# Optimization experiments

Hardware: AMD Instinct MI355X
Metric: run time of the kernel (lower is better)

The kernel has to match this reference:

```python
import jax, jax.numpy as jnp
import numpy as np

N, F, B, D = 16384, 256, 48, 8


def setup_inputs() -> dict:
    key = jax.random.key(0)
    k_x, k_e, k_w, k_b = jax.random.split(key, 4)
    x = jax.random.normal(k_x, (N, F), dtype=jnp.float32)
    # per-feature sorted bin boundaries -> left edges and positive widths
    boundaries = jnp.sort(jax.random.uniform(k_e, (F, B + 1), dtype=jnp.float32,
                                             minval=-3.0, maxval=3.0), axis=-1)
    edges = boundaries[:, :-1]                     # [F, B]
    width = jnp.diff(boundaries, axis=-1)          # [F, B], > 0
    bound = 1.0 / np.sqrt(B)                       # nn.Linear default init
    W = jax.random.uniform(k_w, (F, B, D), dtype=jnp.float32, minval=-bound, maxval=bound)
    b = jax.random.uniform(k_b, (F, D), dtype=jnp.float32, minval=-bound, maxval=bound)
    return {"x": x, "edges": edges, "width": width, "W": W, "b": b}


def reference(x, edges, width, W, b):
    # piecewise-linear encoding: [N, F, B]
    h = (x[:, :, None] - edges) / width
    h = jnp.concatenate([
        jnp.minimum(h[..., :1], 1.0),          # first bin: clamp_max(1)
        jnp.clip(h[..., 1:-1], 0.0, 1.0),      # middle bins: clamp(0, 1)
        jnp.maximum(h[..., -1:], 0.0),         # last bin: clamp_min(0)
    ], axis=-1)
    # per-feature tiny Linear(B -> D), then concat over features
    out = jnp.einsum('nfb,fbd->nfd', h, W) + b   # [N, F, D]
    return out.reshape(x.shape[0], -1)           # [N, F*D]
```

## Files before the change

### kernel.cpp

```cpp
#include <hip/hip_runtime.h>


#define NN 16384
#define FF 256
#define BB 48
#define DD 8

#define FT 8
#define NSPLIT 64
#define NPB (NN / NSPLIT)

#define ESTR 52
#define RASTR 100
#define CSTR 396

__global__ __launch_bounds__(256, 6)
void cple_kernel(const float* __restrict__ X,
                 const float* __restrict__ Edg,
                 const float* __restrict__ Wid,
                 const float* __restrict__ W,
                 const float* __restrict__ Bias,
                 float* __restrict__ Out)
{
    __shared__ float sE [FT * ESTR];
    __shared__ float sRA[FT * RASTR];
    __shared__ float sC [FT * CSTR];

    const int tid = threadIdx.x;
    const int f0  = blockIdx.x * FT;
    const int ns  = blockIdx.y;

    if (tid < FT * BB / 4) {
        const float4* E4 = (const float4*)(Edg + (size_t)f0 * BB);
        float4 v = E4[tid];
        int f = tid / 12, j4 = tid % 12;
        *(float4*)&sE[f * ESTR + j4 * 4] = v;
    }
    for (int idx = tid; idx < FT * BB; idx += 256) {
        int f = idx / BB, j = idx - f * BB;
        float e = Edg[(size_t)f0 * BB + idx];
        float w = Wid[(size_t)f0 * BB + idx];
        float r = 1.0f / w;
        sRA[f * RASTR + 2 * j]     = r;
        sRA[f * RASTR + 2 * j + 1] = -e * r;
    }
    {
        const float4* Wt4 = (const float4*)(W + (size_t)f0 * BB * DD);
        #pragma unroll
        for (int q = 0; q < 3; ++q) {
            int idx4 = tid + q * 256;
            float4 v = Wt4[idx4];
            int idx = idx4 * 4;
            int f   = idx / (BB * DD);
            int rem = idx - f * (BB * DD);
            *(float4*)&sC[f * CSTR + DD + rem] = v;
        }
    }
    __syncthreads();

    const int f_l = tid & 7;
    const int n_l = tid >> 3;
    const float* eF  = &sE [f_l * ESTR];
    const float* raF = &sRA[f_l * RASTR];
    const float* cF  = &sC [f_l * CSTR];
    float c4[11];
    #pragma unroll
    for (int m = 0; m < 11; ++m) c4[m] = eF[4 * (m + 1)];

    if (tid < FT * DD) {
        int f = tid >> 3, d = tid & 7;
        float* c = &sC[f * CSTR + d];
        float acc = Bias[(size_t)(f0 + f) * DD + d];
        c[0] = acc;
        #pragma unroll
        for (int ch = 0; ch < 3; ++ch) {
            float w[16];
            #pragma unroll
            for (int j = 0; j < 16; ++j) w[j] = c[(ch * 16 + j + 1) * DD];
            #pragma unroll
            for (int j = 0; j < 16; ++j) { acc += w[j]; c[(ch * 16 + j + 1) * DD] = acc; }
        }
    }
    __syncthreads();

    const float* xp = X + (f0 + f_l);
    float* op = Out + (size_t)(f0 + f_l) * DD;

    const int nbase = ns * NPB + n_l;
    float xa = xp[(size_t)nbase * FF];
    float xb = xp[(size_t)(nbase + 128) * FF];

    #pragma unroll
    for (int i = 0; i < 4; ++i) {
        int na = nbase + i * 32;
        int nb = na + 128;
        float xA = xa, xB = xb;
        if (i < 3) {
            xa = xp[(size_t)(na + 32) * FF];
            xb = xp[(size_t)(na + 160) * FF];
        }

        int ga = 0, gb = 0;
        #pragma unroll
        for (int m = 0; m < 11; ++m) {
            ga += (xA >= c4[m]) ? 1 : 0;
            gb += (xB >= c4[m]) ? 1 : 0;
        }
        int k4a = ga * 4, k4b = gb * 4;

        float4 ea = *(const float4*)(eF + k4a);
        float4 eb = *(const float4*)(eF + k4b);
        int ka = k4a + (xA >= ea.y) + (xA >= ea.z) + (xA >= ea.w);
        int kb = k4b + (xB >= eb.y) + (xB >= eb.z) + (xB >= eb.w);

        float2 raA = *(const float2*)(raF + 2 * ka);
        float2 raB = *(const float2*)(raF + 2 * kb);
        const float* cKa = cF + ka * DD;
        const float* cKb = cF + kb * DD;
        float4 la0 = *(const float4*)(cKa);
        float4 la1 = *(const float4*)(cKa + 4);
        float4 ha0 = *(const float4*)(cKa + 8);
        float4 ha1 = *(const float4*)(cKa + 12);
        float4 lb0 = *(const float4*)(cKb);
        float4 lb1 = *(const float4*)(cKb + 4);
        float4 hb0 = *(const float4*)(cKb + 8);
        float4 hb1 = *(const float4*)(cKb + 12);

        float ta = fmaf(xA, raA.x, raA.y);
        float tb = fmaf(xB, raB.x, raB.y);

        float4 oa0, oa1, ob0, ob1;
        oa0.x = fmaf(ta, ha0.x - la0.x, la0.x);
        oa0.y = fmaf(ta, ha0.y - la0.y, la0.y);
        oa0.z = fmaf(ta, ha0.z - la0.z, la0.z);
        oa0.w = fmaf(ta, ha0.w - la0.w, la0.w);
        oa1.x = fmaf(ta, ha1.x - la1.x, la1.x);
        oa1.y = fmaf(ta, ha1.y - la1.y, la1.y);
        oa1.z = fmaf(ta, ha1.z - la1.z, la1.z);
        oa1.w = fmaf(ta, ha1.w - la1.w, la1.w);
        ob0.x = fmaf(tb, hb0.x - lb0.x, lb0.x);
        ob0.y = fmaf(tb, hb0.y - lb0.y, lb0.y);
        ob0.z = fmaf(tb, hb0.z - lb0.z, lb0.z);
        ob0.w = fmaf(tb, hb0.w - lb0.w, lb0.w);
        ob1.x = fmaf(tb, hb1.x - lb1.x, lb1.x);
        ob1.y = fmaf(tb, hb1.y - lb1.y, lb1.y);
        ob1.z = fmaf(tb, hb1.z - lb1.z, lb1.z);
        ob1.w = fmaf(tb, hb1.w - lb1.w, lb1.w);

        float4* oA = (float4*)(op + (size_t)na * (FF * DD));
        float4* oB = (float4*)(op + (size_t)nb * (FF * DD));
        oA[0] = oa0; oA[1] = oa1;
        oB[0] = ob0; oB[1] = ob1;
    }
}

extern "C" void kernel_launch(void* const* d_in, const int* in_sizes, int n_in,
                              void* d_out, int out_size, void* d_ws, size_t ws_size,
                              hipStream_t stream) {
    const float* x     = (const float*)d_in[0];
    const float* edges = (const float*)d_in[1];
    const float* width = (const float*)d_in[2];
    const float* W     = (const float*)d_in[3];
    const float* b     = (const float*)d_in[4];
    float* out = (float*)d_out;

    dim3 grid(FF / FT, NSPLIT);
    cple_kernel<<<grid, 256, 0, stream>>>(x, edges, width, W, b, out);
}
```

Measured before the change: 163.8 us.

## Split each row's 8 outputs across thread pairs and hoist x prefetch before barrier

Each (row, feature) output of 8 floats is now split between two adjacent threads, each writing one float4, so a wavefront's stores cover contiguous 16-byte chunks per lane instead of two float4s per lane. This halves the per-thread LDS table reads and FMAs but doubles the loop trip count and makes the bin search redundant across each thread pair. The first x loads are also issued before the first barrier so their latency overlaps the shared-memory setup.

```diff
diff --git a/kernel.cpp b/kernel.cpp
--- a/kernel.cpp
+++ b/kernel.cpp
@@ -56,10 +56,20 @@
             *(float4*)&sC[f * CSTR + DD + rem] = v;
         }
     }
+
+    const int h   = tid & 1;
+    const int f_l = (tid >> 1) & 7;
+    const int n_l = tid >> 4;
+
+    const float* xp = X + (f0 + f_l);
+    float* op = Out + (size_t)(f0 + f_l) * DD + h * 4;
+
+    const int nbase = ns * NPB + n_l;
+    float xa = xp[(size_t)nbase * FF];
+    float xb = xp[(size_t)(nbase + 128) * FF];
+
     __syncthreads();
 
-    const int f_l = tid & 7;
-    const int n_l = tid >> 3;
     const float* eF  = &sE [f_l * ESTR];
     const float* raF = &sRA[f_l * RASTR];
     const float* cF  = &sC [f_l * CSTR];
@@ -83,21 +93,14 @@
     }
     __syncthreads();
 
-    const float* xp = X + (f0 + f_l);
-    float* op = Out + (size_t)(f0 + f_l) * DD;
-
-    const int nbase = ns * NPB + n_l;
-    float xa = xp[(size_t)nbase * FF];
-    float xb = xp[(size_t)(nbase + 128) * FF];
-
     #pragma unroll
-    for (int i = 0; i < 4; ++i) {
-        int na = nbase + i * 32;
+    for (int i = 0; i < 8; ++i) {
+        int na = nbase + i * 16;
         int nb = na + 128;
         float xA = xa, xB = xb;
-        if (i < 3) {
-            xa = xp[(size_t)(na + 32) * FF];
-            xb = xp[(size_t)(na + 160) * FF];
+        if (i < 7) {
+            xa = xp[(size_t)(na + 16) * FF];
+            xb = xp[(size_t)(nb + 16) * FF];
         }
 
         int ga = 0, gb = 0;
@@ -115,42 +118,28 @@
 
         float2 raA = *(const float2*)(raF + 2 * ka);
         float2 raB = *(const float2*)(raF + 2 * kb);
-        const float* cKa = cF + ka * DD;
-        const float* cKb = cF + kb * DD;
-        float4 la0 = *(const float4*)(cKa);
-        float4 la1 = *(const float4*)(cKa + 4);
-        float4 ha0 = *(const float4*)(cKa + 8);
-        float4 ha1 = *(const float4*)(cKa + 12);
-        float4 lb0 = *(const float4*)(cKb);
-        float4 lb1 = *(const float4*)(cKb + 4);
-        float4 hb0 = *(const float4*)(cKb + 8);
-        float4 hb1 = *(const float4*)(cKb + 12);
+        const float* cKa = cF + ka * DD + h * 4;
+        const float* cKb = cF + kb * DD + h * 4;
+        float4 la = *(const float4*)(cKa);
+        float4 ha = *(const float4*)(cKa + DD);
+        float4 lb = *(const float4*)(cKb);
+        float4 hb = *(const float4*)(cKb + DD);
 
         float ta = fmaf(xA, raA.x, raA.y);
         float tb = fmaf(xB, raB.x, raB.y);
 
-        float4 oa0, oa1, ob0, ob1;
-        oa0.x = fmaf(ta, ha0.x - la0.x, la0.x);
-        oa0.y = fmaf(ta, ha0.y - la0.y, la0.y);
-        oa0.z = fmaf(ta, ha0.z - la0.z, la0.z);
-        oa0.w = fmaf(ta, ha0.w - la0.w, la0.w);
-        oa1.x = fmaf(ta, ha1.x - la1.x, la1.x);
-        oa1.y = fmaf(ta, ha1.y - la1.y, la1.y);
-        oa1.z = fmaf(ta, ha1.z - la1.z, la1.z);
-        oa1.w = fmaf(ta, ha1.w - la1.w, la1.w);
-        ob0.x = fmaf(tb, hb0.x - lb0.x, lb0.x);
-        ob0.y = fmaf(tb, hb0.y - lb0.y, lb0.y);
-        ob0.z = fmaf(tb, hb0.z - lb0.z, lb0.z);
-        ob0.w = fmaf(tb, hb0.w - lb0.w, lb0.w);
-        ob1.x = fmaf(tb, hb1.x - lb1.x, lb1.x);
-        ob1.y = fmaf(tb, hb1.y - lb1.y, lb1.y);
-        ob1.z = fmaf(tb, hb1.z - lb1.z, lb1.z);
-        ob1.w = fmaf(tb, hb1.w - lb1.w, lb1.w);
+        float4 oa, ob;
+        oa.x = fmaf(ta, ha.x - la.x, la.x);
+        oa.y = fmaf(ta, ha.y - la.y, la.y);
+        oa.z = fmaf(ta, ha.z - la.z, la.z);
+        oa.w = fmaf(ta, ha.w - la.w, la.w);
+        ob.x = fmaf(tb, hb.x - lb.x, lb.x);
+        ob.y = fmaf(tb, hb.y - lb.y, lb.y);
+        ob.z = fmaf(tb, hb.z - lb.z, lb.z);
+        ob.w = fmaf(tb, hb.w - lb.w, lb.w);
 
-        float4* oA = (float4*)(op + (size_t)na * (FF * DD));
-        float4* oB = (float4*)(op + (size_t)nb * (FF * DD));
-        oA[0] = oa0; oA[1] = oa1;
-        oB[0] = ob0; oB[1] = ob1;
+        *(float4*)(op + (size_t)na * (FF * DD)) = oa;
+        *(float4*)(op + (size_t)nb * (FF * DD)) = ob;
     }
 }
 
```

After: 166.3 us. No clear change (+1.5%).
